# Optimization experiments

Hardware: AMD Instinct MI355X
Metric: run time of the kernel (lower is better)

Reference implementation:

```python
import jax, jax.numpy as jnp
import numpy as np

D = 768      # hidden_size
H = 12       # num_attention_heads
HD = D // H  # head_dim
B, S = 1, 4096


def setup_inputs() -> dict:
    key = jax.random.key(0)
    ks = jax.random.split(key, 9)
    s_in = 1.0 / np.sqrt(D)
    s_o = 1.0 / np.sqrt(D)
    x = jax.random.normal(ks[0], (B, S, D), dtype=jnp.float32)
    # per-head Q/K/V projections stacked: [H, D, HD]
    Wq = jax.random.uniform(ks[1], (H, D, HD), jnp.float32, -s_in, s_in)
    Wk = jax.random.uniform(ks[2], (H, D, HD), jnp.float32, -s_in, s_in)
    Wv = jax.random.uniform(ks[3], (H, D, HD), jnp.float32, -s_in, s_in)
    bq = jax.random.uniform(ks[4], (H, HD), jnp.float32, -s_in, s_in)
    bk = jax.random.uniform(ks[5], (H, HD), jnp.float32, -s_in, s_in)
    bv = jax.random.uniform(ks[6], (H, HD), jnp.float32, -s_in, s_in)
    Wo = jax.random.uniform(ks[7], (D, D), jnp.float32, -s_o, s_o)
    bo = jax.random.uniform(ks[8], (D,), jnp.float32, -s_o, s_o)
    return {"hidden_states": x, "Wq": Wq, "Wk": Wk, "Wv": Wv,
            "bq": bq, "bk": bk, "bv": bv, "Wo": Wo, "bo": bo}


def reference(hidden_states, Wq, Wk, Wv, bq, bk, bv, Wo, bo):
    x = hidden_states  # [B, S, D]
    # fused per-head projections -> [B, H, S, HD]
    q = jnp.einsum('bsd,hde->bhse', x, Wq) + bq[None, :, None, :]
    k = jnp.einsum('bsd,hde->bhse', x, Wk) + bk[None, :, None, :]
    v = jnp.einsum('bsd,hde->bhse', x, Wv) + bv[None, :, None, :]
    scale = 1.0 / jnp.sqrt(jnp.asarray(HD, q.dtype))
    scores = jnp.einsum('bhse,bhte->bhst', q, k) * scale  # [B, H, S, S]
    weights = jax.nn.softmax(scores, axis=-1)
    attn = jnp.einsum('bhst,bhte->bhse', weights, v)  # [B, H, S, HD]
    # concat heads along feature dim -> [B, S, D]
    concat = attn.transpose(0, 2, 1, 3).reshape(x.shape[0], x.shape[1], H * HD)
    return concat @ Wo + bo
```

## Files before the change

### kernel.cpp

```cpp
#include <hip/hip_runtime.h>

#define SLEN 4096
#define DMODEL 768
#define NH 12
#define HD 64
#define NQKV 2304
#define KDIM 768
#define KVBLK 64
#define NT (SLEN / KVBLK)

typedef _Float16 f16x8 __attribute__((ext_vector_type(8)));
typedef _Float16 f16x4v __attribute__((ext_vector_type(4)));
typedef float f32x4 __attribute__((ext_vector_type(4)));
typedef float f32x16 __attribute__((ext_vector_type(16)));

__device__ __forceinline__ void async16(void* lds, const void* g) {
  __builtin_amdgcn_global_load_lds((const __attribute__((address_space(1))) void*)g,
                                   (__attribute__((address_space(3))) void*)lds, 16, 0, 0);
}

__device__ __forceinline__ void plswap(unsigned& a, unsigned& b) {
  auto r = __builtin_amdgcn_permlane32_swap(a, b, false, false);
  a = r[0];
  b = r[1];
}

__device__ __forceinline__ unsigned pk(float a, float b) {
  auto r = __builtin_amdgcn_cvt_pkrtz(a, b);
  return __builtin_bit_cast(unsigned, r);
}

__global__ __launch_bounds__(256) void pack_kernel(
    const float* __restrict__ x, const float* __restrict__ Wq, const float* __restrict__ Wk,
    const float* __restrict__ Wv, const float* __restrict__ Wo,
    _Float16* __restrict__ xb, _Float16* __restrict__ wqkvt, _Float16* __restrict__ wot) {
  int tid = blockIdx.x * 256 + threadIdx.x;
  int stride = gridDim.x * 256;
  int n4 = SLEN * DMODEL / 4;
  for (int i = tid; i < n4; i += stride) {
    float4 v = ((const float4*)x)[i];
    f16x4v o = {(_Float16)v.x, (_Float16)v.y, (_Float16)v.z, (_Float16)v.w};
    ((f16x4v*)xb)[i] = o;
  }
  n4 = NQKV * DMODEL / 4;
  for (int i = tid; i < n4; i += stride) {
    int col = i / (DMODEL / 4);
    int d = (i - col * (DMODEL / 4)) * 4;
    int which = col / DMODEL;
    int cc = col - which * DMODEL;
    int h = cc >> 6, e = cc & 63;
    const float* W = which == 0 ? Wq : (which == 1 ? Wk : Wv);
    const float* s = W + (h * DMODEL + d) * HD + e;
    f16x4v o = {(_Float16)s[0], (_Float16)s[HD], (_Float16)s[2 * HD], (_Float16)s[3 * HD]};
    ((f16x4v*)wqkvt)[i] = o;
  }
  n4 = DMODEL * DMODEL / 4;
  for (int i = tid; i < n4; i += stride) {
    int o_ = i / (DMODEL / 4);
    int d = (i - o_ * (DMODEL / 4)) * 4;
    const float* s = Wo + d * DMODEL + o_;
    f16x4v o = {(_Float16)s[0], (_Float16)s[DMODEL], (_Float16)s[2 * DMODEL], (_Float16)s[3 * DMODEL]};
    ((f16x4v*)wot)[i] = o;
  }
}

__device__ __forceinline__ void gemm_core(const _Float16* __restrict__ A,
                                          const _Float16* __restrict__ Bt,
                                          _Float16* As, _Float16* Bs,
                                          f32x4 (&acc)[4][4], int m0, int n0) {
  int t = threadIdx.x;
  int lane = t & 63, w = t >> 6;
  int lr = lane & 15, lg = lane >> 4;
  int wr = w >> 1, wc = w & 1;
  for (int kb = 0; kb < KDIM / 64; ++kb) {
    #pragma unroll
    for (int i = 0; i < 4; ++i) {
      int base = (w * 4 + i) * 512;
      int off = base + lane * 8;
      int row = off >> 6, col = off & 63;
      async16(&As[base], A + (m0 + row) * KDIM + kb * 64 + col);
      async16(&Bs[base], Bt + (n0 + row) * KDIM + kb * 64 + col);
    }
    __syncthreads();
    #pragma unroll
    for (int kk = 0; kk < 2; ++kk) {
      f16x8 af[4], bf[4];
      #pragma unroll
      for (int mi = 0; mi < 4; ++mi)
        af[mi] = *(const f16x8*)&As[(wr * 64 + mi * 16 + lr) * 64 + kk * 32 + lg * 8];
      #pragma unroll
      for (int ni = 0; ni < 4; ++ni)
        bf[ni] = *(const f16x8*)&Bs[(wc * 64 + ni * 16 + lr) * 64 + kk * 32 + lg * 8];
      #pragma unroll
      for (int mi = 0; mi < 4; ++mi)
        #pragma unroll
        for (int ni = 0; ni < 4; ++ni)
          acc[mi][ni] = __builtin_amdgcn_mfma_f32_16x16x32_f16(af[mi], bf[ni], acc[mi][ni], 0, 0, 0);
    }
    __syncthreads();
  }
}

__global__ __launch_bounds__(256) void gemm_qkv(
    const _Float16* __restrict__ xb, const _Float16* __restrict__ wqkvt,
    const float* __restrict__ bq, const float* __restrict__ bk, const float* __restrict__ bv,
    _Float16* __restrict__ qd, _Float16* __restrict__ kd, _Float16* __restrict__ vtd) {
  __shared__ __align__(16) _Float16 As[128 * 64];
  __shared__ __align__(16) _Float16 Bs[128 * 64];
  f32x4 acc[4][4] = {};
  int m0 = blockIdx.y * 128, n0 = blockIdx.x * 128;
  gemm_core(xb, wqkvt, As, Bs, acc, m0, n0);
  int t = threadIdx.x, lane = t & 63, w = t >> 6;
  int lr = lane & 15, lg = lane >> 4;
  int wr = w >> 1, wc = w & 1;
  int which = n0 / DMODEL;
  const float* bias = which == 0 ? bq : (which == 1 ? bk : bv);
  #pragma unroll
  for (int mi = 0; mi < 4; ++mi)
    #pragma unroll
    for (int ni = 0; ni < 4; ++ni)
      #pragma unroll
      for (int r = 0; r < 4; ++r) {
        int srow = m0 + wr * 64 + mi * 16 + lg * 4 + r;
        int col = n0 + wc * 64 + ni * 16 + lr;
        int cc = col - which * DMODEL;
        int h = cc >> 6, e = cc & 63;
        float val = acc[mi][ni][r] + bias[cc];
        if (which < 2) {
          (which ? kd : qd)[h * (SLEN * HD) + srow * HD + e] = (_Float16)val;
        } else {
          vtd[h * (SLEN * HD) + e * SLEN + srow] = (_Float16)val;
        }
      }
}

__global__ __launch_bounds__(256, 3) void attn_kernel(
    const _Float16* __restrict__ qd, const _Float16* __restrict__ kd,
    const _Float16* __restrict__ vtd, _Float16* __restrict__ attn) {
  __shared__ __align__(16) _Float16 Ks[2][KVBLK * HD];
  __shared__ __align__(16) _Float16 Vts[2][HD * KVBLK];
  __shared__ float Om[2][64][32];
  __shared__ float Mm[2][32], Lm[2][32];
  int wg = blockIdx.x;
  int orig = (wg & 7) * 96 + (wg >> 3);
  int qb = orig & 63, h = orig >> 6;
  int t = threadIdx.x, lane = t & 63, w = t >> 6;
  int wq = w & 1, wk = w >> 1;
  int ql = lane & 31, hi = lane >> 5;

  const _Float16* kbase = kd + h * (SLEN * HD);
  const _Float16* vbase = vtd + h * (SLEN * HD);

  auto stage = [&](int bi, int jb) {
    #pragma unroll
    for (int i = 0; i < 2; ++i) {
      int c = (w * 2 + i) * 64 + lane;
      int row = c >> 3;
      int sb = ((c & 7) * 16) ^ ((row & 7) << 4);
      async16(&Ks[bi][(w * 2 + i) * 512], kbase + (jb * KVBLK + row) * HD + sb / 2);
      async16(&Vts[bi][(w * 2 + i) * 512], vbase + row * SLEN + jb * KVBLK + sb / 2);
    }
  };

  int qrow = qb * 64 + wq * 32 + ql;
  const _Float16* qp = qd + h * (SLEN * HD) + qrow * HD;
  f16x8 qf[4];
  #pragma unroll
  for (int dblk = 0; dblk < 4; ++dblk)
    qf[dblk] = *(const f16x8*)(qp + dblk * 16 + hi * 8);

  f32x16 oacc[2] = {};
  float mrow = -1e30f, lrow = 0.f;
  const float C = 0.18033688f;
  const float THR = 44.4f;

  stage(0, 0);
  __syncthreads();
  int buf = 0;
  for (int jb = 0; jb < NT; ++jb) {
    if (jb + 1 < NT) stage(buf ^ 1, jb + 1);

    f32x16 sacc = {};
    __builtin_amdgcn_s_setprio(1);
    #pragma unroll
    for (int dblk = 0; dblk < 4; ++dblk) {
      int off = ((wk * 32 + ql) * 128 + dblk * 32 + hi * 16) ^ ((ql & 7) << 4);
      f16x8 kf = *(const f16x8*)((const char*)Ks[buf] + off);
      sacc = __builtin_amdgcn_mfma_f32_32x32x16_f16(kf, qf[dblk], sacc, 0, 0, 0);
    }
    __builtin_amdgcn_s_setprio(0);

    float mb = sacc[0];
    #pragma unroll
    for (int r = 1; r < 16; ++r) mb = fmaxf(mb, sacc[r]);
    {
      unsigned a = __builtin_bit_cast(unsigned, mb), b = a;
      plswap(a, b);
      mb = fmaxf(__builtin_bit_cast(float, a), __builtin_bit_cast(float, b));
    }
    if (!__all(mb <= mrow + THR)) {
      float mn = fmaxf(mrow, mb);
      float corr = __builtin_amdgcn_exp2f((mrow - mn) * C);
      lrow *= corr;
      #pragma unroll
      for (int r = 0; r < 16; ++r) { oacc[0][r] *= corr; oacc[1][r] *= corr; }
      mrow = mn;
    }
    float negm = -mrow * C;
    float p[16], ps = 0.f;
    #pragma unroll
    for (int r = 0; r < 16; ++r) { p[r] = __builtin_amdgcn_exp2f(fmaf(sacc[r], C, negm)); ps += p[r]; }
    lrow += ps;

    f16x8 pb[2];
    #pragma unroll
    for (int u = 0; u < 2; ++u) {
      unsigned a0 = pk(p[8 * u + 0], p[8 * u + 1]);
      unsigned b0 = pk(p[8 * u + 4], p[8 * u + 5]);
      unsigned a1 = pk(p[8 * u + 2], p[8 * u + 3]);
      unsigned b1 = pk(p[8 * u + 6], p[8 * u + 7]);
      plswap(a0, b0);
      plswap(a1, b1);
      union { unsigned wd[4]; f16x8 v; } uu;
      uu.wd[0] = a0; uu.wd[1] = a1; uu.wd[2] = b0; uu.wd[3] = b1;
      pb[u] = uu.v;
    }

    __builtin_amdgcn_s_setprio(1);
    #pragma unroll
    for (int u = 0; u < 2; ++u)
      #pragma unroll
      for (int eblk = 0; eblk < 2; ++eblk) {
        int off = ((eblk * 32 + ql) * 128 + wk * 64 + u * 32 + hi * 16) ^ ((ql & 7) << 4);
        f16x8 vf = *(const f16x8*)((const char*)Vts[buf] + off);
        oacc[eblk] = __builtin_amdgcn_mfma_f32_32x32x16_f16(vf, pb[u], oacc[eblk], 0, 0, 0);
      }
    __builtin_amdgcn_s_setprio(0);
    __syncthreads();
    buf ^= 1;
  }

  {
    unsigned a = __builtin_bit_cast(unsigned, lrow), b = a;
    plswap(a, b);
    lrow = __builtin_bit_cast(float, a) + __builtin_bit_cast(float, b);
  }

  if (wk == 1) {
    Mm[wq][ql] = mrow;
    Lm[wq][ql] = lrow;
    #pragma unroll
    for (int eblk = 0; eblk < 2; ++eblk)
      #pragma unroll
      for (int r = 0; r < 16; ++r) {
        int e = eblk * 32 + (r & 3) + 8 * (r >> 2) + 4 * hi;
        Om[wq][e][ql] = oacc[eblk][r];
      }
  }
  __syncthreads();
  if (wk == 0) {
    float m1 = Mm[wq][ql], l1 = Lm[wq][ql];
    float m = fmaxf(mrow, m1);
    float c0 = __builtin_amdgcn_exp2f((mrow - m) * C);
    float c1 = __builtin_amdgcn_exp2f((m1 - m) * C);
    float inv = 1.f / (lrow * c0 + l1 * c1);
    _Float16* ob = attn + qrow * DMODEL + h * HD;
    #pragma unroll
    for (int eblk = 0; eblk < 2; ++eblk) {
      float om[16];
      #pragma unroll
      for (int r = 0; r < 16; ++r) {
        int e = eblk * 32 + (r & 3) + 8 * (r >> 2) + 4 * hi;
        om[r] = (oacc[eblk][r] * c0 + Om[wq][e][ql] * c1) * inv;
      }
      #pragma unroll
      for (int i = 0; i < 4; ++i) {
        unsigned w0 = pk(om[4 * i + 0], om[4 * i + 1]);
        unsigned w1 = pk(om[4 * i + 2], om[4 * i + 3]);
        union { unsigned wd[2]; f16x4v v; } uu;
        uu.wd[0] = w0; uu.wd[1] = w1;
        *(f16x4v*)(ob + eblk * 32 + 8 * i + 4 * hi) = uu.v;
      }
    }
  }
}

__global__ __launch_bounds__(256) void gemm_out(
    const _Float16* __restrict__ attn, const _Float16* __restrict__ wot,
    const float* __restrict__ bo, float* __restrict__ out) {
  __shared__ __align__(16) _Float16 As[128 * 64];
  __shared__ __align__(16) _Float16 Bs[128 * 64];
  f32x4 acc[4][4] = {};
  int m0 = blockIdx.y * 128, n0 = blockIdx.x * 128;
  gemm_core(attn, wot, As, Bs, acc, m0, n0);
  int t = threadIdx.x, lane = t & 63, w = t >> 6;
  int lr = lane & 15, lg = lane >> 4;
  int wr = w >> 1, wc = w & 1;
  #pragma unroll
  for (int mi = 0; mi < 4; ++mi)
    #pragma unroll
    for (int ni = 0; ni < 4; ++ni)
      #pragma unroll
      for (int r = 0; r < 4; ++r) {
        int srow = m0 + wr * 64 + mi * 16 + lg * 4 + r;
        int col = n0 + wc * 64 + ni * 16 + lr;
        out[srow * DMODEL + col] = acc[mi][ni][r] + bo[col];
      }
}

extern "C" void kernel_launch(void* const* d_in, const int* in_sizes, int n_in,
                              void* d_out, int out_size, void* d_ws, size_t ws_size,
                              hipStream_t stream) {
  const float* x  = (const float*)d_in[0];
  const float* Wq = (const float*)d_in[1];
  const float* Wk = (const float*)d_in[2];
  const float* Wv = (const float*)d_in[3];
  const float* bq = (const float*)d_in[4];
  const float* bk = (const float*)d_in[5];
  const float* bv = (const float*)d_in[6];
  const float* Wo = (const float*)d_in[7];
  const float* bo = (const float*)d_in[8];
  float* out = (float*)d_out;

  char* ws = (char*)d_ws;
  size_t off = 0;
  auto alloc = [&](size_t bytes) {
    char* p = ws + off;
    off += (bytes + 255) & ~size_t(255);
    return p;
  };
  _Float16* xb    = (_Float16*)alloc((size_t)SLEN * DMODEL * 2);
  _Float16* wqkvt = (_Float16*)alloc((size_t)NQKV * DMODEL * 2);
  _Float16* wot   = (_Float16*)alloc((size_t)DMODEL * DMODEL * 2);
  _Float16* qd    = (_Float16*)alloc((size_t)NH * SLEN * HD * 2);
  _Float16* kd    = (_Float16*)alloc((size_t)NH * SLEN * HD * 2);
  _Float16* vtd   = (_Float16*)alloc((size_t)NH * SLEN * HD * 2);
  _Float16* attn  = (_Float16*)alloc((size_t)SLEN * DMODEL * 2);

  hipLaunchKernelGGL(pack_kernel, dim3(1024), dim3(256), 0, stream,
                     x, Wq, Wk, Wv, Wo, xb, wqkvt, wot);
  hipLaunchKernelGGL(gemm_qkv, dim3(NQKV / 128, SLEN / 128), dim3(256), 0, stream,
                     xb, wqkvt, bq, bk, bv, qd, kd, vtd);
  hipLaunchKernelGGL(attn_kernel, dim3(768), dim3(256), 0, stream,
                     qd, kd, vtd, attn);
  hipLaunchKernelGGL(gemm_out, dim3(DMODEL / 128, SLEN / 128), dim3(256), 0, stream,
                     attn, wot, bo, out);
}
```

Measured before the change: 242.1 us.

## Alias attention merge buffers onto KV LDS and retile output GEMM to 64x64

The attention kernel now reuses the K/V staging shared memory for the cross-wave merge of partial outputs, cutting its LDS footprint, and raises the launch-bounds occupancy hint from 3 to 5 blocks. The output projection GEMM moves from 128x128 to 64x64 tiles with its own simple single-buffer loop, launching 768 workgroups with an XCD-aware remap instead of 192 blocks. The aim is more resident waves in attention and better CU fill for the small output GEMM. In exchange, attention gets fewer registers per thread and may spill, and the new GEMM loop has no load/compute overlap and less data reuse per tile.

```diff
diff --git a/kernel.cpp b/kernel.cpp
--- a/kernel.cpp
+++ b/kernel.cpp
@@ -134,13 +134,11 @@
       }
 }
 
-__global__ __launch_bounds__(256, 3) void attn_kernel(
+__global__ __launch_bounds__(256, 5) void attn_kernel(
     const _Float16* __restrict__ qd, const _Float16* __restrict__ kd,
     const _Float16* __restrict__ vtd, _Float16* __restrict__ attn) {
   __shared__ __align__(16) _Float16 Ks[2][KVBLK * HD];
   __shared__ __align__(16) _Float16 Vts[2][HD * KVBLK];
-  __shared__ float Om[2][64][32];
-  __shared__ float Mm[2][32], Lm[2][32];
   int wg = blockIdx.x;
   int orig = (wg & 7) * 96 + (wg >> 3);
   int qb = orig & 63, h = orig >> 6;
@@ -246,20 +244,23 @@
     lrow = __builtin_bit_cast(float, a) + __builtin_bit_cast(float, b);
   }
 
+  float* Om = (float*)&Ks[0][0];
+  float* Mm = (float*)&Vts[0][0];
+  float* Lm = Mm + 64;
   if (wk == 1) {
-    Mm[wq][ql] = mrow;
-    Lm[wq][ql] = lrow;
+    Mm[wq * 32 + ql] = mrow;
+    Lm[wq * 32 + ql] = lrow;
     #pragma unroll
     for (int eblk = 0; eblk < 2; ++eblk)
       #pragma unroll
       for (int r = 0; r < 16; ++r) {
         int e = eblk * 32 + (r & 3) + 8 * (r >> 2) + 4 * hi;
-        Om[wq][e][ql] = oacc[eblk][r];
+        Om[(wq * 64 + e) * 32 + ql] = oacc[eblk][r];
       }
   }
   __syncthreads();
   if (wk == 0) {
-    float m1 = Mm[wq][ql], l1 = Lm[wq][ql];
+    float m1 = Mm[wq * 32 + ql], l1 = Lm[wq * 32 + ql];
     float m = fmaxf(mrow, m1);
     float c0 = __builtin_amdgcn_exp2f((mrow - m) * C);
     float c1 = __builtin_amdgcn_exp2f((m1 - m) * C);
@@ -271,7 +272,7 @@
       #pragma unroll
       for (int r = 0; r < 16; ++r) {
         int e = eblk * 32 + (r & 3) + 8 * (r >> 2) + 4 * hi;
-        om[r] = (oacc[eblk][r] * c0 + Om[wq][e][ql] * c1) * inv;
+        om[r] = (oacc[eblk][r] * c0 + Om[(wq * 64 + e) * 32 + ql] * c1) * inv;
       }
       #pragma unroll
       for (int i = 0; i < 4; ++i) {
@@ -288,22 +289,51 @@
 __global__ __launch_bounds__(256) void gemm_out(
     const _Float16* __restrict__ attn, const _Float16* __restrict__ wot,
     const float* __restrict__ bo, float* __restrict__ out) {
-  __shared__ __align__(16) _Float16 As[128 * 64];
-  __shared__ __align__(16) _Float16 Bs[128 * 64];
-  f32x4 acc[4][4] = {};
-  int m0 = blockIdx.y * 128, n0 = blockIdx.x * 128;
-  gemm_core(attn, wot, As, Bs, acc, m0, n0);
+  __shared__ __align__(16) _Float16 As[64 * 64];
+  __shared__ __align__(16) _Float16 Bs[64 * 64];
+  f32x4 acc[2][2] = {};
+  int wg = blockIdx.x;
+  int orig = (wg & 7) * 96 + (wg >> 3);
+  int mb = orig / 12, nb = orig - mb * 12;
+  int m0 = mb * 64, n0 = nb * 64;
   int t = threadIdx.x, lane = t & 63, w = t >> 6;
   int lr = lane & 15, lg = lane >> 4;
   int wr = w >> 1, wc = w & 1;
+  for (int kb = 0; kb < KDIM / 64; ++kb) {
+    #pragma unroll
+    for (int i = 0; i < 2; ++i) {
+      int base = (w * 2 + i) * 512;
+      int off = base + lane * 8;
+      int row = off >> 6, col = off & 63;
+      async16(&As[base], attn + (m0 + row) * DMODEL + kb * 64 + col);
+      async16(&Bs[base], wot + (n0 + row) * DMODEL + kb * 64 + col);
+    }
+    __syncthreads();
+    #pragma unroll
+    for (int kk = 0; kk < 2; ++kk) {
+      f16x8 af[2], bf[2];
+      #pragma unroll
+      for (int mi = 0; mi < 2; ++mi)
+        af[mi] = *(const f16x8*)&As[(wr * 32 + mi * 16 + lr) * 64 + kk * 32 + lg * 8];
+      #pragma unroll
+      for (int ni = 0; ni < 2; ++ni)
+        bf[ni] = *(const f16x8*)&Bs[(wc * 32 + ni * 16 + lr) * 64 + kk * 32 + lg * 8];
+      #pragma unroll
+      for (int mi = 0; mi < 2; ++mi)
+        #pragma unroll
+        for (int ni = 0; ni < 2; ++ni)
+          acc[mi][ni] = __builtin_amdgcn_mfma_f32_16x16x32_f16(af[mi], bf[ni], acc[mi][ni], 0, 0, 0);
+    }
+    __syncthreads();
+  }
   #pragma unroll
-  for (int mi = 0; mi < 4; ++mi)
-    #pragma unroll
-    for (int ni = 0; ni < 4; ++ni)
+  for (int mi = 0; mi < 2; ++mi)
+    #pragma unroll
+    for (int ni = 0; ni < 2; ++ni)
       #pragma unroll
       for (int r = 0; r < 4; ++r) {
-        int srow = m0 + wr * 64 + mi * 16 + lg * 4 + r;
-        int col = n0 + wc * 64 + ni * 16 + lr;
+        int srow = m0 + wr * 32 + mi * 16 + lg * 4 + r;
+        int col = n0 + wc * 32 + ni * 16 + lr;
         out[srow * DMODEL + col] = acc[mi][ni][r] + bo[col];
       }
 }
@@ -343,6 +373,6 @@
                      xb, wqkvt, bq, bk, bv, qd, kd, vtd);
   hipLaunchKernelGGL(attn_kernel, dim3(768), dim3(256), 0, stream,
                      qd, kd, vtd, attn);
-  hipLaunchKernelGGL(gemm_out, dim3(DMODEL / 128, SLEN / 128), dim3(256), 0, stream,
+  hipLaunchKernelGGL(gemm_out, dim3(768), dim3(256), 0, stream,
                      attn, wot, bo, out);
 }
```

Result: faster. 237.0 us (-2.1%).
